# Kernel tuning notes

Hardware: AMD Instinct MI355X
Metric: run time of the kernel (lower is better)

Reference implementation:

```python
import jax, jax.numpy as jnp
import numpy as np

N_GRAMS = 3
N_KERNELS = 11

def _kernel_mus(K):
    l = [1.0]
    if K == 1:
        return l
    bs = 2.0 / (K - 1)
    l.append(1.0 - bs / 2.0)
    for i in range(1, K - 1):
        l.append(l[i] - bs)
    return l

def _kernel_sigmas(K):
    if K == 1:
        return [0.001]
    bs = 2.0 / (K - 1)
    return [0.001] + [0.5 * bs] * (K - 1)

MU = jnp.asarray(_kernel_mus(N_KERNELS), jnp.float32)       # (K,)
SIGMA = jnp.asarray(_kernel_sigmas(N_KERNELS), jnp.float32)  # (K,)

def _conv_relu(x, w, b):
    # x: (B,E,L), w: (O,E,h); right-pad h-1 so output length == L (as ConstantPad1d((0,h-1)))
    h = w.shape[-1]
    y = jax.lax.conv_general_dilated(x, w, (1,), [(0, h - 1)], dimension_numbers=('NCH', 'OIH', 'NCH'))
    return jax.nn.relu(y + b[None, :, None]).transpose(0, 2, 1)  # (B,L,O)

def _cosine(a, b):
    # CosineMatrixAttention: normalize rows then matmul
    an = a / (jnp.linalg.norm(a, axis=-1, keepdims=True) + 1e-13)
    bn = b / (jnp.linalg.norm(b, axis=-1, keepdims=True) + 1e-13)
    return jnp.einsum('bqe,bde->bqd', an, bn)

def setup_inputs() -> dict:
    key = jax.random.key(0)
    ks = jax.random.split(key, 12)
    B, Lq, Ld, V, E, O = 128, 64, 512, 30000, 300, 128
    inp = {}
    inp['tokens_q'] = jax.random.randint(ks[0], (B, Lq), 0, V)
    inp['tokens_d'] = jax.random.randint(ks[1], (B, Ld), 0, V)
    inp['emb'] = jax.random.normal(ks[2], (V, E), jnp.float32) * 0.1
    for i, h in enumerate((1, 2, 3)):
        inp['conv_w%d' % h] = jax.random.normal(ks[3 + i], (O, E, h), jnp.float32) * (1.0 / np.sqrt(E * h))
        inp['conv_b%d' % h] = jnp.zeros((O,), jnp.float32)
    inp['fc_w'] = jax.random.normal(ks[9], (1, N_KERNELS * N_GRAMS * N_GRAMS), jnp.float32) * 0.1
    inp['fc_b'] = jnp.zeros((1,), jnp.float32)
    return inp

def reference(tokens_q, tokens_d, emb, conv_w1, conv_b1, conv_w2, conv_b2, conv_w3, conv_b3, fc_w, fc_b):
    qmask = (tokens_q > 0).astype(jnp.float32)  # (B,Lq)
    dmask = (tokens_d > 0).astype(jnp.float32)  # (B,Ld)
    qe = emb[tokens_q].transpose(0, 2, 1)  # (B,E,Lq)
    de = emb[tokens_d].transpose(0, 2, 1)  # (B,E,Ld)
    cws = [(conv_w1, conv_b1), (conv_w2, conv_b2), (conv_w3, conv_b3)]
    hq = [_conv_relu(qe, w, b) for w, b in cws]  # each (B,Lq,O)
    hd = [_conv_relu(de, w, b) for w, b in cws]  # each (B,Ld,O)
    pair_mask = qmask[:, :, None] * dmask[:, None, :]  # (B,Lq,Ld)
    mu = MU[None, None, None, :]
    sig = SIGMA[None, None, None, :]
    feats = []
    for q in range(N_GRAMS):
        for d in range(N_GRAMS):
            m = _cosine(hq[q], hd[d]) * pair_mask  # (B,Lq,Ld)
            rbf = jnp.exp(-jnp.square(m[..., None] - mu) / (2.0 * jnp.square(sig))) * pair_mask[..., None]
            qk = rbf.sum(axis=2)  # (B,Lq,K)
            logk = jnp.log(jnp.maximum(qk, 1e-10)) * 0.01
            # NOTE: original has a typo (loq_ vs log_) so the query mask is NOT applied before summing
            feats.append(logk.sum(axis=1))  # (B,K)
    cross = jnp.concatenate(feats, axis=-1)  # (B, K*G*G)
    return cross @ fc_w.T + fc_b  # (B,1)
```

## Files before the change

### kernel.cpp

```cpp
#include <hip/hip_runtime.h>
#include <hip/hip_bf16.h>

typedef __attribute__((ext_vector_type(8))) short short8;
typedef __attribute__((ext_vector_type(4))) float f32x4;

#define E_DIM 300
#define NCH   128
#define NOUT  384
#define NCHUNK 30

__device__ __forceinline__ unsigned short f2bf(float f) {
    unsigned int u = __float_as_uint(f);
    u += 0x7FFFu + ((u >> 16) & 1u);
    return (unsigned short)(u >> 16);
}
__device__ __forceinline__ float bf2f(unsigned short s) {
    return __uint_as_float(((unsigned int)s) << 16);
}

__global__ void pack_wb(const float* __restrict__ w1, const float* __restrict__ w2,
                        const float* __restrict__ w3, unsigned short* __restrict__ Wp) {
    int idx = blockIdx.x * 256 + threadIdx.x;
    if (idx >= NCHUNK * NOUT * 32) return;
    int ke = idx & 31;
    int n  = (idx >> 5) % NOUT;
    int c  = idx / (32 * NOUT);
    int s  = c / 10;
    int e  = (c % 10) * 32 + ke;
    int g  = n >> 7, o = n & 127, h = g + 1;
    float v = 0.0f;
    if (e < E_DIM && s < h) {
        const float* w = (g == 0) ? w1 : ((g == 1) ? w2 : w3);
        v = w[(o * E_DIM + e) * h + s];
    }
    Wp[idx] = f2bf(v);
}

__launch_bounds__(512, 4)
__global__ void conv_mfma(const int* __restrict__ tokens_q, const int* __restrict__ tokens_d,
                          const float* __restrict__ emb, const unsigned short* __restrict__ Wp,
                          const float* __restrict__ b1, const float* __restrict__ b2,
                          const float* __restrict__ b3,
                          unsigned short* __restrict__ hq, unsigned short* __restrict__ hd) {
    __shared__ __align__(16) short xs[66 * 320];
    __shared__ float nrm[64 * 3];

    int bx   = blockIdx.x;
    int b    = bx / 9;
    int tile = bx % 9;
    int isq  = (tile == 0);
    int L    = isq ? 64 : 512;
    int t0   = isq ? 0 : (tile - 1) * 64;
    const int* toks = isq ? (tokens_q + b * 64) : (tokens_d + b * 512);
    int tid  = threadIdx.x;
    int lane = tid & 63;
    int wn   = tid >> 6;
    int lr   = lane & 15;
    int lg   = lane >> 4;

    if (tid < 192) nrm[tid] = 0.0f;

    for (int i = tid; i < 66 * 80; i += 512) {
        int r   = i / 80;
        int f4  = i - r * 80;
        int byt = (f4 * 8) ^ ((r & 7) << 4);
        ushort4 u = {0, 0, 0, 0};
        int pos = t0 + r;
        if (f4 < 75 && pos < L) {
            int tk = toks[pos];
            float4 v = *(const float4*)(emb + (size_t)tk * E_DIM + f4 * 4);
            u.x = f2bf(v.x); u.y = f2bf(v.y); u.z = f2bf(v.z); u.w = f2bf(v.w);
        }
        *(ushort4*)((char*)xs + r * 640 + byt) = u;
    }
    __syncthreads();

    f32x4 acc[4][3];
    #pragma unroll
    for (int i = 0; i < 4; ++i)
        #pragma unroll
        for (int g = 0; g < 3; ++g) acc[i][g] = (f32x4){0.f, 0.f, 0.f, 0.f};

    const unsigned short* __restrict__ wpB = Wp + (size_t)(wn * 16 + lr) * 32 + lg * 8;
    short8 bbc[3], bbn[3];

#define LOADB(dst, c, g) dst = *(const short8*)(wpB + (size_t)((c) * NOUT + (g) * 128) * 32)

#define PHASE(S) { \
    _Pragma("unroll") for (int g = (S); g < 3; ++g) { LOADB(bbc[g], (S) * 10, g); } \
    _Pragma("unroll") \
    for (int ec = 0; ec < 10; ++ec) { \
        if (ec < 9) { _Pragma("unroll") for (int g = (S); g < 3; ++g) { LOADB(bbn[g], (S) * 10 + ec + 1, g); } } \
        short8 a[4]; \
        _Pragma("unroll") for (int i = 0; i < 4; ++i) { \
            int row = i * 16 + lr + (S); \
            int byt = (ec * 64 + lg * 16) ^ ((row & 7) << 4); \
            a[i] = *(const short8*)((const char*)xs + row * 640 + byt); \
        } \
        _Pragma("unroll") for (int i = 0; i < 4; ++i) \
            _Pragma("unroll") for (int g = (S); g < 3; ++g) \
                acc[i][g] = __builtin_amdgcn_mfma_f32_16x16x32_bf16(a[i], bbc[g], acc[i][g], 0, 0, 0); \
        if (ec < 9) { _Pragma("unroll") for (int g = (S); g < 3; ++g) bbc[g] = bbn[g]; } \
    } }

    PHASE(0)
    PHASE(1)
    PHASE(2)
#undef PHASE
#undef LOADB

    #pragma unroll
    for (int g = 0; g < 3; ++g) {
        float bv = (g == 0 ? b1 : (g == 1 ? b2 : b3))[wn * 16 + lr];
        #pragma unroll
        for (int i = 0; i < 4; ++i)
            #pragma unroll
            for (int r = 0; r < 4; ++r) {
                float v = acc[i][g][r] + bv;
                v = v > 0.0f ? v : 0.0f;
                acc[i][g][r] = v;
                float s = v * v;
                s += __shfl_xor(s, 1, 16);
                s += __shfl_xor(s, 2, 16);
                s += __shfl_xor(s, 4, 16);
                s += __shfl_xor(s, 8, 16);
                if (lr == 0) atomicAdd(&nrm[(i * 16 + lg * 4 + r) * 3 + g], s);
            }
    }
    __syncthreads();

    unsigned short* outp = isq ? hq : hd;
    #pragma unroll
    for (int g = 0; g < 3; ++g) {
        #pragma unroll
        for (int i = 0; i < 4; ++i)
            #pragma unroll
            for (int r = 0; r < 4; ++r) {
                int row = i * 16 + lg * 4 + r;
                float inv = 1.0f / (sqrtf(nrm[row * 3 + g]) + 1e-13f);
                outp[((size_t)(g * 128 + b) * L + t0 + row) * NCH + wn * 16 + lr] =
                    f2bf(acc[i][g][r] * inv);
            }
    }
}

#define QPITCH 136
__launch_bounds__(256, 3)
__global__ void sim_rbf(const unsigned short* __restrict__ hq,
                        const unsigned short* __restrict__ hd,
                        const int* __restrict__ tokens_q, const int* __restrict__ tokens_d,
                        float* __restrict__ cross) {
    __shared__ __align__(16) short qs[64 * QPITCH];
    __shared__ __align__(16) short ds2[2][64 * QPITCH];
    __shared__ unsigned char dm_s[512];
    __shared__ float logk_s[11];

    int bx = blockIdx.x;
    int b  = bx / 9;
    int p  = bx % 9;
    int gq = p / 3;
    int gd = p % 3;
    int tid = threadIdx.x;
    int lane = tid & 63;
    int wn   = tid >> 6;
    int lr   = lane & 15;
    int lg   = lane >> 4;

    if (tid < 11) logk_s[tid] = 0.0f;
    for (int i = tid; i < 512; i += 256)
        dm_s[i] = (tokens_d[b * 512 + i] > 0) ? 1 : 0;

    const unsigned short* qsrc = hq + ((size_t)(gq * 128 + b) * 64) * NCH;
    const unsigned short* dsrc = hd + ((size_t)(gd * 128 + b) * 512) * NCH;

    #pragma unroll
    for (int it = 0; it < 4; ++it) {
        int row  = it * 16 + (tid >> 4);
        int col8 = (tid & 15) * 8;
        *(uint4*)&qs[row * QPITCH + col8] = *(const uint4*)&qsrc[row * NCH + col8];
    }
    #pragma unroll
    for (int it = 0; it < 4; ++it) {
        int row  = it * 16 + (tid >> 4);
        int col8 = (tid & 15) * 8;
        *(uint4*)&ds2[0][row * QPITCH + col8] = *(const uint4*)&dsrc[row * NCH + col8];
    }
    __syncthreads();

    int q  = wn * 16 + lr;
    float qm = (tokens_q[b * 64 + q] > 0) ? 1.0f : 0.0f;

    short8 qf[4];
    #pragma unroll
    for (int ks = 0; ks < 4; ++ks)
        qf[ks] = *(const short8*)&qs[(wn * 16 + lr) * QPITCH + ks * 32 + lg * 8];

    float qk[11];
    #pragma unroll
    for (int k = 0; k < 11; ++k) qk[k] = 0.0f;

    const float C4 = 0.0183156389f;

    for (int ch = 0; ch < 8; ++ch) {
        int buf = ch & 1;
        uint4 r4[4];
        if (ch < 7) {
            #pragma unroll
            for (int it = 0; it < 4; ++it) {
                int row  = it * 16 + (tid >> 4);
                int col8 = (tid & 15) * 8;
                r4[it] = *(const uint4*)&dsrc[((size_t)(ch + 1) * 64 + row) * NCH + col8];
            }
        }

        #pragma unroll
        for (int mt = 0; mt < 4; ++mt) {
            f32x4 acc = (f32x4){0.f, 0.f, 0.f, 0.f};
            #pragma unroll
            for (int ks = 0; ks < 4; ++ks) {
                short8 a = *(const short8*)&ds2[buf][(mt * 16 + lr) * QPITCH + ks * 32 + lg * 8];
                acc = __builtin_amdgcn_mfma_f32_16x16x32_bf16(a, qf[ks], acc, 0, 0, 0);
            }
            uchar4 du = *(const uchar4*)&dm_s[ch * 64 + mt * 16 + lg * 4];
            float cv[4], cm[4];
            cm[0] = qm * (float)du.x; cm[1] = qm * (float)du.y;
            cm[2] = qm * (float)du.z; cm[3] = qm * (float)du.w;
            #pragma unroll
            for (int r = 0; r < 4; ++r) cv[r] = acc[r] * cm[r];

            float cmx = fmaxf(fmaxf(cv[0], cv[1]), fmaxf(cv[2], cv[3]));
            if (__any(cmx > 0.98f)) {
                #pragma unroll
                for (int r = 0; r < 4; ++r) {
                    if (cv[r] > 0.98f) {
                        float t0 = cv[r] - 1.0f;
                        qk[0] += __expf(-500000.0f * t0 * t0);
                    }
                }
            }
            #pragma unroll
            for (int r = 0; r < 4; ++r) {
                float c  = cv[r];
                float tA = c - 0.1f;
                float TA = __expf(-50.0f * tA * tA) * cm[r];
                float UA = __expf(20.0f * c - 4.0f);
                float tB = c + 0.1f;
                float TB = __expf(-50.0f * tB * tB) * cm[r];
                float UB = __expf(-20.0f * c - 4.0f);
                qk[5] += TA;
                TA *= UA; qk[4] += TA; UA *= C4;
                TA *= UA; qk[3] += TA; UA *= C4;
                TA *= UA; qk[2] += TA; UA *= C4;
                TA *= UA; qk[1] += TA;
                qk[6] += TB;
                TB *= UB; qk[7] += TB; UB *= C4;
                TB *= UB; qk[8] += TB; UB *= C4;
                TB *= UB; qk[9] += TB; UB *= C4;
                TB *= UB; qk[10] += TB;
            }
        }

        if (ch < 7) {
            #pragma unroll
            for (int it = 0; it < 4; ++it) {
                int row  = it * 16 + (tid >> 4);
                int col8 = (tid & 15) * 8;
                *(uint4*)&ds2[buf ^ 1][row * QPITCH + col8] = r4[it];
            }
        }
        __syncthreads();
    }

    #pragma unroll
    for (int k = 0; k < 11; ++k) {
        float v = qk[k];
        v += __shfl_xor(v, 16);
        v += __shfl_xor(v, 32);
        qk[k] = v;
    }
    if (lg == 0) {
        #pragma unroll
        for (int k = 0; k < 11; ++k) {
            float lv = __logf(fmaxf(qk[k], 1e-10f)) * 0.01f;
            atomicAdd(&logk_s[k], lv);
        }
    }
    __syncthreads();
    if (tid < 11) cross[b * 99 + p * 11 + tid] = logk_s[tid];
}

__global__ void fc_kernel(const float* __restrict__ cross, const float* __restrict__ fc_w,
                          const float* __restrict__ fc_b, float* __restrict__ out) {
    int b = threadIdx.x;
    float acc = fc_b[0];
    #pragma unroll 11
    for (int j = 0; j < 99; ++j) acc += cross[b * 99 + j] * fc_w[j];
    out[b] = acc;
}

extern "C" void kernel_launch(void* const* d_in, const int* in_sizes, int n_in,
                              void* d_out, int out_size, void* d_ws, size_t ws_size,
                              hipStream_t stream) {
    const int*   tq  = (const int*)d_in[0];
    const int*   td  = (const int*)d_in[1];
    const float* emb = (const float*)d_in[2];
    const float* w1  = (const float*)d_in[3];
    const float* cb1 = (const float*)d_in[4];
    const float* w2  = (const float*)d_in[5];
    const float* cb2 = (const float*)d_in[6];
    const float* w3  = (const float*)d_in[7];
    const float* cb3 = (const float*)d_in[8];
    const float* fcw = (const float*)d_in[9];
    const float* fcb = (const float*)d_in[10];

    char* ws = (char*)d_ws;
    unsigned short* Wp    = (unsigned short*)ws;
    float*          cross = (float*)(ws + 921600);
    unsigned short* hq    = (unsigned short*)(ws + 1048576);
    unsigned short* hd    = (unsigned short*)(ws + 8388608);

    hipLaunchKernelGGL(pack_wb, dim3(1440), dim3(256), 0, stream, w1, w2, w3, Wp);
    hipLaunchKernelGGL(conv_mfma, dim3(128 * 9), dim3(512), 0, stream,
                       tq, td, emb, Wp, cb1, cb2, cb3, hq, hd);
    hipLaunchKernelGGL(sim_rbf, dim3(128 * 9), dim3(256), 0, stream, hq, hd, tq, td, cross);
    hipLaunchKernelGGL(fc_kernel, dim3(1), dim3(128), 0, stream, cross, fcw, fcb, (float*)d_out);
}
```

Before: 206.5 us.

## Stage conv outputs through LDS for coalesced stores and restructure B prefetch

The conv kernel now writes its normalized bf16 outputs into shared memory first, then stores them to global memory as 8-byte vectors instead of scattered 2-byte writes. The embedding tile layout changes from an XOR swizzle to a padded pitch. The three unrolled phases become one 30-chunk loop with a double-buffered weight prefetch two chunks ahead, and the first two weight chunks are loaded before the embedding gather. The aim is better global store coalescing and weight loads that overlap the gather; the cost is an extra barrier and LDS round trip, plus possible bank conflicts from the padded pitch.

Result: no change. 207.1 us (+0.3%).

```diff
diff --git a/kernel.cpp b/kernel.cpp
--- a/kernel.cpp
+++ b/kernel.cpp
@@ -9,13 +9,13 @@
 #define NOUT  384
 #define NCHUNK 30
 
+#define APITCH 656
+#define OPITCH 792
+
 __device__ __forceinline__ unsigned short f2bf(float f) {
     unsigned int u = __float_as_uint(f);
     u += 0x7FFFu + ((u >> 16) & 1u);
     return (unsigned short)(u >> 16);
-}
-__device__ __forceinline__ float bf2f(unsigned short s) {
-    return __uint_as_float(((unsigned int)s) << 16);
 }
 
 __global__ void pack_wb(const float* __restrict__ w1, const float* __restrict__ w2,
@@ -42,7 +42,7 @@
                           const float* __restrict__ b1, const float* __restrict__ b2,
                           const float* __restrict__ b3,
                           unsigned short* __restrict__ hq, unsigned short* __restrict__ hd) {
-    __shared__ __align__(16) short xs[66 * 320];
+    __shared__ __align__(16) char lds[64 * OPITCH];
     __shared__ float nrm[64 * 3];
 
     int bx   = blockIdx.x;
@@ -60,10 +60,17 @@
 
     if (tid < 192) nrm[tid] = 0.0f;
 
+    const unsigned short* __restrict__ wpB = Wp + (size_t)(wn * 16 + lr) * 32 + lg * 8;
+    short8 bb[2][3];
+    #pragma unroll
+    for (int g = 0; g < 3; ++g) {
+        bb[0][g] = *(const short8*)(wpB + (size_t)(0 * NOUT + g * 128) * 32);
+        bb[1][g] = *(const short8*)(wpB + (size_t)(1 * NOUT + g * 128) * 32);
+    }
+
     for (int i = tid; i < 66 * 80; i += 512) {
         int r   = i / 80;
         int f4  = i - r * 80;
-        int byt = (f4 * 8) ^ ((r & 7) << 4);
         ushort4 u = {0, 0, 0, 0};
         int pos = t0 + r;
         if (f4 < 75 && pos < L) {
@@ -71,7 +78,7 @@
             float4 v = *(const float4*)(emb + (size_t)tk * E_DIM + f4 * 4);
             u.x = f2bf(v.x); u.y = f2bf(v.y); u.z = f2bf(v.z); u.w = f2bf(v.w);
         }
-        *(ushort4*)((char*)xs + r * 640 + byt) = u;
+        *(ushort4*)(lds + r * APITCH + f4 * 8) = u;
     }
     __syncthreads();
 
@@ -81,33 +88,28 @@
         #pragma unroll
         for (int g = 0; g < 3; ++g) acc[i][g] = (f32x4){0.f, 0.f, 0.f, 0.f};
 
-    const unsigned short* __restrict__ wpB = Wp + (size_t)(wn * 16 + lr) * 32 + lg * 8;
-    short8 bbc[3], bbn[3];
-
-#define LOADB(dst, c, g) dst = *(const short8*)(wpB + (size_t)((c) * NOUT + (g) * 128) * 32)
-
-#define PHASE(S) { \
-    _Pragma("unroll") for (int g = (S); g < 3; ++g) { LOADB(bbc[g], (S) * 10, g); } \
-    _Pragma("unroll") \
-    for (int ec = 0; ec < 10; ++ec) { \
-        if (ec < 9) { _Pragma("unroll") for (int g = (S); g < 3; ++g) { LOADB(bbn[g], (S) * 10 + ec + 1, g); } } \
-        short8 a[4]; \
-        _Pragma("unroll") for (int i = 0; i < 4; ++i) { \
-            int row = i * 16 + lr + (S); \
-            int byt = (ec * 64 + lg * 16) ^ ((row & 7) << 4); \
-            a[i] = *(const short8*)((const char*)xs + row * 640 + byt); \
-        } \
-        _Pragma("unroll") for (int i = 0; i < 4; ++i) \
-            _Pragma("unroll") for (int g = (S); g < 3; ++g) \
-                acc[i][g] = __builtin_amdgcn_mfma_f32_16x16x32_bf16(a[i], bbc[g], acc[i][g], 0, 0, 0); \
-        if (ec < 9) { _Pragma("unroll") for (int g = (S); g < 3; ++g) bbc[g] = bbn[g]; } \
-    } }
-
-    PHASE(0)
-    PHASE(1)
-    PHASE(2)
-#undef PHASE
-#undef LOADB
+    const char* abase = lds + lr * APITCH + lg * 16;
+
+    #pragma unroll
+    for (int c = 0; c < NCHUNK; ++c) {
+        const int S  = (c >= 20) ? 2 : ((c >= 10) ? 1 : 0);
+        const int ec = c - S * 10;
+        short8 a[4];
+        #pragma unroll
+        for (int i = 0; i < 4; ++i)
+            a[i] = *(const short8*)(abase + (i * 16 + S) * APITCH + ec * 64);
+        #pragma unroll
+        for (int i = 0; i < 4; ++i)
+            #pragma unroll
+            for (int g = S; g < 3; ++g)
+                acc[i][g] = __builtin_amdgcn_mfma_f32_16x16x32_bf16(a[i], bb[c & 1][g], acc[i][g], 0, 0, 0);
+        if (c < NCHUNK - 2) {
+            const int S2 = ((c + 2) >= 20) ? 2 : (((c + 2) >= 10) ? 1 : 0);
+            #pragma unroll
+            for (int g = S2; g < 3; ++g)
+                bb[c & 1][g] = *(const short8*)(wpB + (size_t)((c + 2) * NOUT + g * 128) * 32);
+        }
+    }
 
     #pragma unroll
     for (int g = 0; g < 3; ++g) {
@@ -129,18 +131,30 @@
     }
     __syncthreads();
 
+    unsigned short* os = (unsigned short*)lds;
+    #pragma unroll
+    for (int i = 0; i < 4; ++i)
+        #pragma unroll
+        for (int r = 0; r < 4; ++r) {
+            int row = i * 16 + lg * 4 + r;
+            #pragma unroll
+            for (int g = 0; g < 3; ++g) {
+                float inv = 1.0f / (sqrtf(nrm[row * 3 + g]) + 1e-13f);
+                os[row * (OPITCH / 2) + g * 128 + wn * 16 + lr] = f2bf(acc[i][g][r] * inv);
+            }
+        }
+    __syncthreads();
+
     unsigned short* outp = isq ? hq : hd;
     #pragma unroll
-    for (int g = 0; g < 3; ++g) {
-        #pragma unroll
-        for (int i = 0; i < 4; ++i)
-            #pragma unroll
-            for (int r = 0; r < 4; ++r) {
-                int row = i * 16 + lg * 4 + r;
-                float inv = 1.0f / (sqrtf(nrm[row * 3 + g]) + 1e-13f);
-                outp[((size_t)(g * 128 + b) * L + t0 + row) * NCH + wn * 16 + lr] =
-                    f2bf(acc[i][g][r] * inv);
-            }
+    for (int it = 0; it < 12; ++it) {
+        int idx = it * 512 + tid;
+        int row = idx / 96;
+        int c8  = idx - row * 96;
+        int g   = c8 >> 5;
+        int ch  = (c8 & 31) * 4;
+        uint2 v = *(const uint2*)(lds + row * OPITCH + c8 * 8);
+        *(uint2*)&outp[((size_t)(g * 128 + b) * L + t0 + row) * NCH + ch] = v;
     }
 }
 
```
